# Performance work log

Measured on AMD Instinct MI355X. Metric: run time of the kernel, lower is better.

## Reference

```python
import jax, jax.numpy as jnp
import numpy as np
from math import factorial

IRREPS = [0] * 256 + [1] * 256 + [2] * 128 + [3] * 64
N_BATCH, CHANNELS = 1024, 32


def _dfact(n):
    r = 1
    while n > 1:
        r *= n
        n -= 2
    return r


def _sh_l(l, xyz):
    """Real spherical harmonics of degree l, components m=-l..l, at unit vectors xyz."""
    x, y, z = xyz[:, 0], xyz[:, 1], xyz[:, 2]
    phi = np.arctan2(y, x)
    ct = z
    st = np.sqrt(np.clip(1.0 - ct * ct, 0.0, None))
    Y = np.zeros((xyz.shape[0], 2 * l + 1))
    for m in range(l + 1):
        pmm = ((-1.0) ** m) * _dfact(2 * m - 1) * st ** m  # P_m^m(cos t)
        if l == m:
            plm = pmm
        else:
            pm1 = ct * (2 * m + 1) * pmm  # P_{m+1}^m
            if l == m + 1:
                plm = pm1
            else:
                p2, p1 = pmm, pm1
                for ll in range(m + 2, l + 1):
                    p2, p1 = p1, ((2 * ll - 1) * ct * p1 - (ll + m - 1) * p2) / (ll - m)
                plm = p1
        K = np.sqrt((2 * l + 1) / (4 * np.pi) * factorial(l - m) / factorial(l + m))
        if m == 0:
            Y[:, l] = K * plm
        else:
            Y[:, l + m] = np.sqrt(2.0) * K * np.cos(m * phi) * plm
            Y[:, l - m] = np.sqrt(2.0) * K * np.sin(m * phi) * plm
    return Y


def _j_matrix(l):
    """Orthogonal involution J_l: real-SH matrix of the y<->z axis swap (J = J^T = J^-1)."""
    rng = np.random.default_rng(0)
    v = rng.normal(size=(max(256, 16 * (2 * l + 1)), 3))
    v /= np.linalg.norm(v, axis=1, keepdims=True)
    A = _sh_l(l, v)
    B = _sh_l(l, v[:, [0, 2, 1]])  # Y(swap r)
    X, _, _, _ = np.linalg.lstsq(A, B, rcond=None)
    return X.T  # Y(swap r) = J @ Y(r)


def _build_info():
    freq, rev, groups = [], [], []
    off = 0
    i = 0
    while i < len(IRREPS):
        l = IRREPS[i]
        mul = 0
        while i < len(IRREPS) and IRREPS[i] == l:
            mul += 1
            i += 1
        d = 2 * l + 1
        groups.append((l, off, mul, np.asarray(_j_matrix(l), np.float32)))
        for _ in range(mul):
            for k in range(d):
                freq.append(k - l)      # m value of component k
                rev.append(off + (d - 1 - k))  # index of the -m partner
            off += d
    return np.asarray(freq, np.float32), np.asarray(rev, np.int32), groups, off


FREQ_NP, REV_NP, GROUPS, DIM = _build_info()
FREQ = jnp.asarray(FREQ_NP)
REV = jnp.asarray(REV_NP)
J_MATS = [jnp.asarray(J) for (_, _, _, J) in GROUPS]


def _z_rot(x, theta):
    """Per-m z-rotation (sparse vecsca): out_m = cos(m t) x_m - sin(m t) x_{-m}."""
    ang = theta[:, None] * FREQ  # (N, DIM)
    return jnp.cos(ang)[..., None] * x - jnp.sin(ang)[..., None] * x[:, REV, :]


def _j_apply(x):
    """Block-diagonal J application, grouped by l (sparse scale / flip stage)."""
    n, _, c = x.shape
    outs = []
    for (l, off, mul, _), J in zip(GROUPS, J_MATS):
        d = 2 * l + 1
        seg = x[:, off:off + mul * d, :].reshape(n, mul, d, c)
        outs.append(jnp.einsum('pq,nmqc->nmpc', J, seg).reshape(n, mul * d, c))
    return jnp.concatenate(outs, axis=1)


def setup_inputs() -> dict:
    key = jax.random.key(0)
    k0, k1, k2, k3 = jax.random.split(key, 4)
    two_pi = 2.0 * np.pi
    return {
        'input': jax.random.normal(k0, (N_BATCH, DIM, CHANNELS), dtype=jnp.float32),
        'alpha': jax.random.uniform(k1, (N_BATCH,), dtype=jnp.float32) * two_pi,
        'beta': jax.random.uniform(k2, (N_BATCH,), dtype=jnp.float32) * two_pi,
        'gamma': jax.random.uniform(k3, (N_BATCH,), dtype=jnp.float32) * two_pi,
    }


def reference(input, alpha, beta, gamma):
    # D(alpha, beta, gamma) = Dz(alpha) J Dz(beta) J Dz(gamma)
    x = _z_rot(input, gamma)
    x = _j_apply(x)
    x = _z_rot(x, beta)
    x = _j_apply(x)
    return _z_rot(x, alpha)
```

## Files before the change

kernel.cpp:

```cpp
#include <hip/hip_runtime.h>
#include <math.h>


namespace {

typedef float f4 __attribute__((ext_vector_type(4)));

constexpr float SQ3_2 = 0.86602540378443864676f;
constexpr float S6    = 0.61237243569579452455f;
constexpr float S10   = 0.79056941504209483300f;
constexpr float S15   = 0.96824583655185422129f;

template<int L> struct JM;
template<> struct JM<1> {
  static constexpr float v[3][3] = {
    { 0.f, -1.f, 0.f},
    {-1.f,  0.f, 0.f},
    { 0.f,  0.f, 1.f}};
};
template<> struct JM<2> {
  static constexpr float v[5][5] = {
    { 0.f, 0.f,  0.f,   -1.f,  0.f},
    { 0.f, 1.f,  0.f,    0.f,  0.f},
    { 0.f, 0.f, -0.5f,   0.f, -SQ3_2},
    {-1.f, 0.f,  0.f,    0.f,  0.f},
    { 0.f, 0.f, -SQ3_2,  0.f,  0.5f}};
};
template<> struct JM<3> {
  static constexpr float v[7][7] = {
    { 0.f, 0.f, 0.f, S10,  0.f,   -S6,  0.f},
    { 0.f, 1.f, 0.f, 0.f,  0.f,    0.f, 0.f},
    { 0.f, 0.f, 0.f, S6,   0.f,    S10, 0.f},
    { S10, 0.f, S6,  0.f,  0.f,    0.f, 0.f},
    { 0.f, 0.f, 0.f, 0.f, -0.25f,  0.f, -S15},
    {-S6,  0.f, S10, 0.f,  0.f,    0.f, 0.f},
    { 0.f, 0.f, 0.f, 0.f, -S15,    0.f, 0.25f}};
};

template<int L>
__device__ inline void compute_M_col(int q, float al, float be, float ga, float* M) {
  constexpr int D = 2 * L + 1;
  const int mq = q - L;
  float sg, cg;
  sincosf((float)mq * ga, &sg, &cg);
  float v[D];
#pragma unroll
  for (int p = 0; p < D; ++p)
    v[p] = cg * JM<L>::v[p][q] + sg * JM<L>::v[p][(D - 1) - q];
  float c1, s1;
  sincosf(be, &s1, &c1);
  float cb[L + 1], sb[L + 1];
  cb[0] = 1.f; sb[0] = 0.f;
  cb[1] = c1;  sb[1] = s1;
#pragma unroll
  for (int k = 2; k <= L; ++k) {
    cb[k] = 2.f * c1 * cb[k - 1] - cb[k - 2];
    sb[k] = 2.f * c1 * sb[k - 1] - sb[k - 2];
  }
  float w[D];
#pragma unroll
  for (int p = 0; p < D; ++p) {
    const int mp = p - L;
    const int am = mp < 0 ? -mp : mp;
    const float c = cb[am];
    const float s = mp < 0 ? -sb[am] : sb[am];
    w[p] = c * v[p] - s * v[(D - 1) - p];
  }
  float u[D];
#pragma unroll
  for (int p = 0; p < D; ++p) {
    float acc = 0.f;
#pragma unroll
    for (int r = 0; r < D; ++r) acc = fmaf(JM<L>::v[p][r], w[r], acc);
    u[p] = acc;
  }
  sincosf(al, &s1, &c1);
  float ca[L + 1], sa[L + 1];
  ca[0] = 1.f; sa[0] = 0.f;
  ca[1] = c1;  sa[1] = s1;
#pragma unroll
  for (int k = 2; k <= L; ++k) {
    ca[k] = 2.f * c1 * ca[k - 1] - ca[k - 2];
    sa[k] = 2.f * c1 * sa[k - 1] - sa[k - 2];
  }
#pragma unroll
  for (int p = 0; p < D; ++p) {
    const int mp = p - L;
    const int am = mp < 0 ? -mp : mp;
    const float c = ca[am];
    const float s = mp < 0 ? -sa[am] : sa[am];
    M[p * D + q] = c * u[p] - s * u[(D - 1) - p];
  }
}

__global__ __launch_bounds__(256) void build_M_kernel(
    const float* __restrict__ alpha, const float* __restrict__ beta,
    const float* __restrict__ gamma, float* __restrict__ ws, int n_batch) {
  const int t = threadIdx.x;
  const int n = blockIdx.x * 16 + (t >> 4);
  const int col = t & 15;
  if (n >= n_batch || col >= 15) return;
  const float al = alpha[n], be = beta[n], ga = gamma[n];
  float* w = ws + (size_t)n * 96;
  if (col < 7)       compute_M_col<3>(col,      al, be, ga, w);
  else if (col < 12) compute_M_col<2>(col - 7,  al, be, ga, w + 49);
  else               compute_M_col<1>(col - 12, al, be, ga, w + 74);
}

__device__ inline float uload(const float* __restrict__ p) {
  return __int_as_float(__builtin_amdgcn_readfirstlane(__float_as_int(*p)));
}

template<int D, int NC>
__device__ inline void apply_unit(const f4* __restrict__ inU,
                                  f4* __restrict__ outU,
                                  const float* __restrict__ Ms,
                                  int g, int ch) {
  const int base = g * (NC * D * 8) + ch;
  f4 v[NC][D];
#pragma unroll
  for (int j = 0; j < NC; ++j)
#pragma unroll
    for (int q = 0; q < D; ++q)
      v[j][q] = __builtin_nontemporal_load(inU + base + (j * D + q) * 8);
  f4 o[NC][D];
#pragma unroll
  for (int j = 0; j < NC; ++j)
#pragma unroll
    for (int p = 0; p < D; ++p) {
      f4 a = Ms[p * D] * v[j][0];
#pragma unroll
      for (int q = 1; q < D; ++q) a += Ms[p * D + q] * v[j][q];
      o[j][p] = a;
    }
#pragma unroll
  for (int j = 0; j < NC; ++j)
#pragma unroll
    for (int p = 0; p < D; ++p)
      __builtin_nontemporal_store(o[j][p], outU + base + (j * D + p) * 8);
}

template<int D>
__device__ inline void run_unit(const f4* __restrict__ inU, f4* __restrict__ outU,
                                const float* __restrict__ ws_n, int moff,
                                int g, int ch) {
  float Ms[D * D];
#pragma unroll
  for (int i = 0; i < D * D; ++i) Ms[i] = uload(ws_n + moff + i);
  constexpr int NC = (D == 3) ? 4 : 2;
  apply_unit<D, NC>(inU, outU, Ms, g, ch);
}

__global__ __launch_bounds__(256) void wigner_stream_kernel(
    const float* __restrict__ in, const float* __restrict__ ws,
    float* __restrict__ out, int n_units, int grid) {
  const int t = threadIdx.x;
  const int g = t >> 3, ch = t & 7;
  for (int u = blockIdx.x; u < n_units; u += grid) {
    const int n = u / 6, k = u - n * 6;
    const size_t base = (size_t)n * 16896;
    const f4* inN = (const f4*)in + base;
    f4* outN = (f4*)out + base;
    const float* ws_n = ws + (size_t)n * 96;
    if (k == 0) {
      f4 c[8];
#pragma unroll
      for (int j = 0; j < 8; ++j)
        c[j] = __builtin_nontemporal_load(inN + t + 256 * j);
#pragma unroll
      for (int j = 0; j < 8; ++j)
        __builtin_nontemporal_store(c[j], outN + t + 256 * j);
    } else if (k <= 2) {
      const int soff = 2048 + (k - 1) * 3072;
      run_unit<3>(inN + soff, outN + soff, ws_n, 74, g, ch);
    } else if (k <= 4) {
      const int soff = 8192 + (k - 3) * 2560;
      run_unit<5>(inN + soff, outN + soff, ws_n, 49, g, ch);
    } else {
      run_unit<7>(inN + 13312, outN + 13312, ws_n, 0, g, ch);
    }
  }
}

}

extern "C" void kernel_launch(void* const* d_in, const int* in_sizes, int n_in,
                              void* d_out, int out_size, void* d_ws, size_t ws_size,
                              hipStream_t stream) {
  const float* in    = (const float*)d_in[0];
  const float* alpha = (const float*)d_in[1];
  const float* beta  = (const float*)d_in[2];
  const float* gamma = (const float*)d_in[3];
  float* out = (float*)d_out;
  const int n_batch = in_sizes[1];

  float* ws = (float*)d_ws;
  build_M_kernel<<<(n_batch + 15) / 16, 256, 0, stream>>>(alpha, beta, gamma,
                                                          ws, n_batch);
  const int n_units = n_batch * 6;
  const int grid = n_units < 1025 ? n_units : 1025;
  wigner_stream_kernel<<<grid, 256, 0, stream>>>(in, ws, out, n_units, grid);
}
```

Baseline: 108.2 us.

## Fuse Wigner matrix construction into streaming kernel via shared memory

Removes the separate build_M kernel launch and its global workspace round-trip. Each block now computes the per-batch rotation matrix for its l-group in shared memory (a few threads run compute_M_col), synchronises, then applies it. It also adds a launch-bounds occupancy hint. In exchange, matrix construction is recomputed per unit, and the two barriers leave most threads idle while a handful of lanes do the trig work, which could add latency to a bandwidth-bound kernel.

```diff
diff --git a/kernel.cpp b/kernel.cpp
--- a/kernel.cpp
+++ b/kernel.cpp
@@ -93,29 +93,15 @@
   }
 }
 
-__global__ __launch_bounds__(256) void build_M_kernel(
-    const float* __restrict__ alpha, const float* __restrict__ beta,
-    const float* __restrict__ gamma, float* __restrict__ ws, int n_batch) {
-  const int t = threadIdx.x;
-  const int n = blockIdx.x * 16 + (t >> 4);
-  const int col = t & 15;
-  if (n >= n_batch || col >= 15) return;
-  const float al = alpha[n], be = beta[n], ga = gamma[n];
-  float* w = ws + (size_t)n * 96;
-  if (col < 7)       compute_M_col<3>(col,      al, be, ga, w);
-  else if (col < 12) compute_M_col<2>(col - 7,  al, be, ga, w + 49);
-  else               compute_M_col<1>(col - 12, al, be, ga, w + 74);
-}
-
-__device__ inline float uload(const float* __restrict__ p) {
+__device__ inline float uflds(const float* __restrict__ p) {
   return __int_as_float(__builtin_amdgcn_readfirstlane(__float_as_int(*p)));
 }
 
 template<int D, int NC>
-__device__ inline void apply_unit(const f4* __restrict__ inU,
-                                  f4* __restrict__ outU,
-                                  const float* __restrict__ Ms,
-                                  int g, int ch) {
+__device__ inline void run_unit(const f4* __restrict__ inU,
+                                f4* __restrict__ outU,
+                                const float* __restrict__ Mlds,
+                                int g, int ch) {
   const int base = g * (NC * D * 8) + ch;
   f4 v[NC][D];
 #pragma unroll
@@ -123,6 +109,9 @@
 #pragma unroll
     for (int q = 0; q < D; ++q)
       v[j][q] = __builtin_nontemporal_load(inU + base + (j * D + q) * 8);
+  float Ms[D * D];
+#pragma unroll
+  for (int i = 0; i < D * D; ++i) Ms[i] = uflds(Mlds + i);
   f4 o[NC][D];
 #pragma unroll
   for (int j = 0; j < NC; ++j)
@@ -140,20 +129,11 @@
       __builtin_nontemporal_store(o[j][p], outU + base + (j * D + p) * 8);
 }
 
-template<int D>
-__device__ inline void run_unit(const f4* __restrict__ inU, f4* __restrict__ outU,
-                                const float* __restrict__ ws_n, int moff,
-                                int g, int ch) {
-  float Ms[D * D];
-#pragma unroll
-  for (int i = 0; i < D * D; ++i) Ms[i] = uload(ws_n + moff + i);
-  constexpr int NC = (D == 3) ? 4 : 2;
-  apply_unit<D, NC>(inU, outU, Ms, g, ch);
-}
-
-__global__ __launch_bounds__(256) void wigner_stream_kernel(
-    const float* __restrict__ in, const float* __restrict__ ws,
+__global__ __launch_bounds__(256, 4) void wigner_kernel(
+    const float* __restrict__ in, const float* __restrict__ alpha,
+    const float* __restrict__ beta, const float* __restrict__ gamma,
     float* __restrict__ out, int n_units, int grid) {
+  __shared__ float Mlds[49];
   const int t = threadIdx.x;
   const int g = t >> 3, ch = t & 7;
   for (int u = blockIdx.x; u < n_units; u += grid) {
@@ -161,7 +141,6 @@
     const size_t base = (size_t)n * 16896;
     const f4* inN = (const f4*)in + base;
     f4* outN = (f4*)out + base;
-    const float* ws_n = ws + (size_t)n * 96;
     if (k == 0) {
       f4 c[8];
 #pragma unroll
@@ -170,14 +149,25 @@
 #pragma unroll
       for (int j = 0; j < 8; ++j)
         __builtin_nontemporal_store(c[j], outN + t + 256 * j);
-    } else if (k <= 2) {
-      const int soff = 2048 + (k - 1) * 3072;
-      run_unit<3>(inN + soff, outN + soff, ws_n, 74, g, ch);
-    } else if (k <= 4) {
-      const int soff = 8192 + (k - 3) * 2560;
-      run_unit<5>(inN + soff, outN + soff, ws_n, 49, g, ch);
     } else {
-      run_unit<7>(inN + 13312, outN + 13312, ws_n, 0, g, ch);
+      __syncthreads();
+      if (k <= 2) {
+        if (t < 3) compute_M_col<1>(t, alpha[n], beta[n], gamma[n], Mlds);
+      } else if (k <= 4) {
+        if (t < 5) compute_M_col<2>(t, alpha[n], beta[n], gamma[n], Mlds);
+      } else {
+        if (t < 7) compute_M_col<3>(t, alpha[n], beta[n], gamma[n], Mlds);
+      }
+      __syncthreads();
+      if (k <= 2) {
+        const int soff = 2048 + (k - 1) * 3072;
+        run_unit<3, 4>(inN + soff, outN + soff, Mlds, g, ch);
+      } else if (k <= 4) {
+        const int soff = 8192 + (k - 3) * 2560;
+        run_unit<5, 2>(inN + soff, outN + soff, Mlds, g, ch);
+      } else {
+        run_unit<7, 2>(inN + 13312, outN + 13312, Mlds, g, ch);
+      }
     }
   }
 }
@@ -194,10 +184,8 @@
   float* out = (float*)d_out;
   const int n_batch = in_sizes[1];
 
-  float* ws = (float*)d_ws;
-  build_M_kernel<<<(n_batch + 15) / 16, 256, 0, stream>>>(alpha, beta, gamma,
-                                                          ws, n_batch);
   const int n_units = n_batch * 6;
   const int grid = n_units < 1025 ? n_units : 1025;
-  wigner_stream_kernel<<<grid, 256, 0, stream>>>(in, ws, out, n_units, grid);
+  wigner_kernel<<<grid, 256, 0, stream>>>(in, alpha, beta, gamma, out,
+                                          n_units, grid);
 }
```

Result: faster. 103.7 us (-4.2%).
